# Performance work log

Measured on AMD Instinct MI355X. Metric: run time of the kernel, lower is better.

The kernel has to match this reference:

```python
import jax, jax.numpy as jnp
import numpy as np

N_NODES = 50000
N_EDGES = 600000
D = 128
LN_EPS = 1e-5


def _mlp_ln(x, W1, b1, W2, b2, g, beta):
    # Linear -> ReLU -> Linear -> LayerNorm (standard MeshGraphNets model_fn)
    h = jax.nn.relu(x @ W1 + b1)
    y = h @ W2 + b2
    mu = jnp.mean(y, axis=-1, keepdims=True)
    var = jnp.var(y, axis=-1, keepdims=True)
    return (y - mu) * jax.lax.rsqrt(var + LN_EPS) * g + beta


def setup_inputs() -> dict:
    key = jax.random.key(0)
    ks = jax.random.split(key, 16)
    def glorot(k, shape):
        fan = shape[0] + shape[1]
        return jax.random.normal(k, shape, jnp.float32) * np.sqrt(2.0 / fan)
    inp = {
        "node_features": jax.random.normal(ks[0], (1, N_NODES, D), jnp.float32),
        "edge_features": jax.random.normal(ks[1], (1, N_EDGES, D), jnp.float32),
        "senders": jax.random.randint(ks[2], (N_EDGES,), 0, N_NODES),
        "receivers": jax.random.randint(ks[3], (N_EDGES,), 0, N_NODES),
        # edge MLP: in 3*D -> 128 -> D, LayerNorm
        "eW1": glorot(ks[4], (3 * D, 128)), "eb1": jnp.zeros((128,), jnp.float32),
        "eW2": glorot(ks[5], (128, D)), "eb2": jnp.zeros((D,), jnp.float32),
        "eg": jnp.ones((D,), jnp.float32), "ebeta": jnp.zeros((D,), jnp.float32),
        # node MLP: in 2*D -> 128 -> D, LayerNorm
        "nW1": glorot(ks[6], (2 * D, 128)), "nb1": jnp.zeros((128,), jnp.float32),
        "nW2": glorot(ks[7], (128, D)), "nb2": jnp.zeros((D,), jnp.float32),
        "ng": jnp.ones((D,), jnp.float32), "nbeta": jnp.zeros((D,), jnp.float32),
        # attention linear D -> 1
        "aW": glorot(ks[8], (D, 1)), "ab": jnp.zeros((1,), jnp.float32),
    }
    return inp


def reference(node_features, edge_features, senders, receivers,
              eW1, eb1, eW2, eb2, eg, ebeta,
              nW1, nb1, nW2, nb2, ng, nbeta,
              aW, ab):
    # --- edge update: gather + concat + MLP ---
    sf = node_features[:, senders]      # [1,E,D]
    rf = node_features[:, receivers]    # [1,E,D]
    new_ef = _mlp_ln(jnp.concatenate([sf, rf, edge_features], -1),
                     eW1, eb1, eW2, eb2, eg, ebeta)  # [1,E,D]
    # --- per-edge attention: linear + LeakyReLU + scatter_softmax over receivers ---
    logits = jax.nn.leaky_relu(new_ef @ aW + ab, 0.2)[0, :, 0]  # [E]
    seg_max = jax.ops.segment_max(logits, receivers, num_segments=N_NODES)
    seg_max = jnp.where(jnp.isfinite(seg_max), seg_max, 0.0)
    ex = jnp.exp(logits - seg_max[receivers])
    seg_sum = jax.ops.segment_sum(ex, receivers, num_segments=N_NODES)
    att = ex / seg_sum[receivers]  # [E]
    # --- scatter-add aggregation ---
    agg = jax.ops.segment_sum(new_ef[0] * att[:, None], receivers,
                              num_segments=N_NODES)[None]  # [1,N,D]
    new_nf = _mlp_ln(jnp.concatenate([node_features, agg], -1),
                     nW1, nb1, nW2, nb2, ng, nbeta)  # [1,N,D]
    # residual connections
    new_nf = new_nf + node_features
    new_ef = new_ef + edge_features
    return new_nf, new_ef
```

## Files before the change

### kernel.cpp

```cpp
#include <hip/hip_runtime.h>
#include <hip/hip_bf16.h>

#define N_NODES 50000
#define N_EDGES 600000
#define D 128
#define LN_EPS 1e-5f

typedef float f32x4 __attribute__((ext_vector_type(4)));
typedef int   i32x4 __attribute__((ext_vector_type(4)));
typedef short s16x8 __attribute__((ext_vector_type(8)));

#define W1P_OFF     0u
#define W2P_OFF     98304u
#define NW1P_OFF    131072u
#define NW2P_OFF    196608u
#define SEGKEY_OFF  229376u
#define SEGSUM_OFF  429440u
#define LOGITS_OFF  629504u
#define EX_OFF      3029504u
#define AGG_OFF     5429504u
#define RAW_OFF     31029504u
#define WS_NEED_RAW (RAW_OFF + (size_t)N_EDGES * D * 2)

static __device__ __forceinline__ unsigned short f2bf(float f) {
    unsigned int u = __float_as_uint(f);
    u = (u + 0x7FFFu + ((u >> 16) & 1u)) >> 16;
    return (unsigned short)u;
}
static __device__ __forceinline__ float bf2f(unsigned short h) {
    unsigned int u = ((unsigned int)h) << 16;
    return __uint_as_float(u);
}
static __device__ __forceinline__ int pkbf2(float a, float b) {
    union { __hip_bfloat16 h[2]; int i; } u;
    u.h[0] = __float2bfloat16(a);
    u.h[1] = __float2bfloat16(b);
    return u.i;
}
union frag_u { i32x4 i; s16x8 s; };
static __device__ __forceinline__ unsigned int fkey(float f) {
    unsigned int u = __float_as_uint(f);
    return (u & 0x80000000u) ? ~u : (u | 0x80000000u);
}
static __device__ __forceinline__ float unkey(unsigned int k) {
    unsigned int u = (k & 0x80000000u) ? (k & 0x7FFFFFFFu) : ~k;
    return __uint_as_float(u);
}
static __device__ __forceinline__ f32x4 mfma_bf16(s16x8 a, s16x8 b, f32x4 c) {
    return __builtin_amdgcn_mfma_f32_16x16x32_bf16(a, b, c, 0, 0, 0);
}

__global__ void k_init(const float* __restrict__ eW1, const float* __restrict__ eW2,
                       const float* __restrict__ nW1, const float* __restrict__ nW2,
                       char* __restrict__ ws) {
    int idx = blockIdx.x * 256 + threadIdx.x;
    if (idx < N_NODES * D) ((float*)(ws + AGG_OFF))[idx] = 0.0f;
    if (idx < N_NODES) {
        ((unsigned int*)(ws + SEGKEY_OFF))[idx] = 0u;
        ((float*)(ws + SEGSUM_OFF))[idx] = 0.0f;
    }
    int e = idx & 7, lane = (idx >> 3) & 63, ct = (idx >> 9) & 7, ks = idx >> 12;
    int k = ks * 32 + (lane >> 4) * 8 + e;
    int j = ct * 16 + (lane & 15);
    if (idx < 12 * 4096) ((unsigned short*)(ws + W1P_OFF))[idx]  = f2bf(eW1[k * 128 + j]);
    if (idx < 4 * 4096)  ((unsigned short*)(ws + W2P_OFF))[idx]  = f2bf(eW2[k * 128 + j]);
    if (idx < 8 * 4096)  ((unsigned short*)(ws + NW1P_OFF))[idx] = f2bf(nW1[k * 128 + j]);
    if (idx < 4 * 4096)  ((unsigned short*)(ws + NW2P_OFF))[idx] = f2bf(nW2[k * 128 + j]);
}

template <int STORE_RAW>
__global__ __launch_bounds__(256, 4) void k_edge(
    const float* __restrict__ nf, const float* __restrict__ ef,
    const int* __restrict__ snd, const int* __restrict__ rcv,
    const i32x4* __restrict__ B1, const i32x4* __restrict__ B2,
    const float* __restrict__ b1, const float* __restrict__ b2,
    const float* __restrict__ g, const float* __restrict__ beta,
    const float* __restrict__ aW, const float* __restrict__ ab,
    float* __restrict__ out_ef, float* __restrict__ logits,
    unsigned int* __restrict__ segkey, unsigned short* __restrict__ rawbuf)
{
    __shared__ __align__(16) char  hbuf[64 * 128 * 2];
    __shared__ __align__(16) i32x4 bstage[2][512];
    const int tid = threadIdx.x, lane = tid & 63, rt = tid >> 6;
    const int j0 = lane & 15, hi = lane >> 4;

    const long eA = (long)blockIdx.x * 64 + rt * 16 + j0;
    const int sA = snd[eA], rA = rcv[eA];
    const float* __restrict__ prowS = nf + (size_t)sA * D;
    const float* __restrict__ prowR = nf + (size_t)rA * D;
    const float* __restrict__ prowE = ef + (size_t)eA * D;

    bstage[0][tid]       = B1[tid];
    bstage[0][256 + tid] = B1[256 + tid];
    __syncthreads();

    f32x4 acc[8];
    #pragma unroll
    for (int ct = 0; ct < 8; ++ct) acc[ct] = (f32x4){0.f, 0.f, 0.f, 0.f};
    for (int s = 0; s < 12; ++s) {
        const int cur = s & 1, nxt = cur ^ 1;
        const i32x4* src = (s + 1 < 12) ? (B1 + (s + 1) * 512) : B2;
        i32x4 t0 = src[tid], t1 = src[256 + tid];
        bstage[nxt][tid]       = t0;
        bstage[nxt][256 + tid] = t1;
        const float* p = (s < 4 ? prowS : (s < 8 ? prowR : prowE)) + (s & 3) * 32 + hi * 8;
        float4 f0 = *(const float4*)p;
        float4 f1 = *(const float4*)(p + 4);
        frag_u a;
        a.i[0] = pkbf2(f0.x, f0.y); a.i[1] = pkbf2(f0.z, f0.w);
        a.i[2] = pkbf2(f1.x, f1.y); a.i[3] = pkbf2(f1.z, f1.w);
        #pragma unroll
        for (int ct = 0; ct < 8; ++ct) {
            frag_u b; b.i = bstage[cur][ct * 64 + lane];
            acc[ct] = mfma_bf16(a.s, b.s, acc[ct]);
        }
        __syncthreads();
    }

    #pragma unroll
    for (int ct = 0; ct < 8; ++ct) {
        float bb = b1[ct * 16 + j0];
        #pragma unroll
        for (int rg = 0; rg < 4; ++rg) {
            int row = rt * 16 + hi * 4 + rg;
            float y = fmaxf(acc[ct][rg] + bb, 0.0f);
            int addr = (row * 256 + (ct * 16 + j0) * 2) ^ ((row & 7) << 4);
            *(__hip_bfloat16*)(hbuf + addr) = __float2bfloat16(y);
        }
    }
    asm volatile("" ::: "memory");

    #pragma unroll
    for (int ct = 0; ct < 8; ++ct) acc[ct] = (f32x4){0.f, 0.f, 0.f, 0.f};
    {
        const int arow = rt * 16 + j0;
        for (int s2 = 0; s2 < 4; ++s2) {
            const int cur = (12 + s2) & 1, nxt = cur ^ 1;
            if (s2 < 3) {
                const i32x4* src = B2 + (s2 + 1) * 512;
                i32x4 t0 = src[tid], t1 = src[256 + tid];
                bstage[nxt][tid]       = t0;
                bstage[nxt][256 + tid] = t1;
            }
            int addr = (arow * 256 + (s2 * 32 + hi * 8) * 2) ^ ((arow & 7) << 4);
            frag_u a;
            a.i = *(const i32x4*)(hbuf + addr);
            #pragma unroll
            for (int ct = 0; ct < 8; ++ct) {
                frag_u b; b.i = bstage[cur][ct * 64 + lane];
                acc[ct] = mfma_bf16(a.s, b.s, acc[ct]);
            }
            if (s2 < 3) __syncthreads();
        }
    }

    float b2v[8], gv[8], bv[8], awv[8];
    #pragma unroll
    for (int ct = 0; ct < 8; ++ct) {
        int c = ct * 16 + j0;
        b2v[ct] = b2[c]; gv[ct] = g[c]; bv[ct] = beta[c]; awv[ct] = aW[c];
    }
    float abv = ab[0];
    #pragma unroll
    for (int rg = 0; rg < 4; ++rg) {
        int row = rt * 16 + hi * 4 + rg;
        long e = (long)blockIdx.x * 64 + row;
        float y[8]; float s = 0.f, sq = 0.f;
        #pragma unroll
        for (int ct = 0; ct < 8; ++ct) {
            y[ct] = acc[ct][rg] + b2v[ct];
            s += y[ct]; sq += y[ct] * y[ct];
        }
        #pragma unroll
        for (int m = 1; m <= 8; m <<= 1) { s += __shfl_xor(s, m); sq += __shfl_xor(sq, m); }
        float mu = s * (1.0f / 128.0f);
        float var = sq * (1.0f / 128.0f) - mu * mu;
        float rs = rsqrtf(var + LN_EPS);
        const float* efr = ef + (size_t)e * D;
        float* outr = out_ef + (size_t)e * D;
        unsigned short* rawr = STORE_RAW ? (rawbuf + (size_t)e * D) : nullptr;
        float lg = 0.f;
        #pragma unroll
        for (int ct = 0; ct < 8; ++ct) {
            int c = ct * 16 + j0;
            float o = (y[ct] - mu) * rs * gv[ct] + bv[ct];
            outr[c] = o + efr[c];
            if (STORE_RAW) rawr[c] = f2bf(o);
            lg += o * awv[ct];
        }
        #pragma unroll
        for (int m = 1; m <= 8; m <<= 1) lg += __shfl_xor(lg, m);
        if (j0 == 0) {
            float L = lg + abv;
            L = (L >= 0.f) ? L : 0.2f * L;
            logits[e] = L;
            atomicMax(&segkey[rcv[e]], fkey(L));
        }
    }
}

__global__ void k_exps(const float* __restrict__ logits, const int* __restrict__ rcv,
                       const unsigned int* __restrict__ segkey,
                       float* __restrict__ ex, float* __restrict__ segsum)
{
    int e = blockIdx.x * 256 + threadIdx.x;
    if (e >= N_EDGES) return;
    int r = rcv[e];
    float v = __expf(logits[e] - unkey(segkey[r]));
    ex[e] = v;
    unsafeAtomicAdd(&segsum[r], v);
}

__global__ void k_scatter_raw(const unsigned short* __restrict__ raw,
                              const int* __restrict__ rcv, const float* __restrict__ ex,
                              const float* __restrict__ segsum, float* __restrict__ agg)
{
    long idx = (long)blockIdx.x * 256 + threadIdx.x;
    int e = (int)(idx >> 7);
    int c = (int)(idx & 127);
    int r = rcv[e];
    float att = ex[e] / segsum[r];
    unsafeAtomicAdd(&agg[(size_t)r * D + c], bf2f(raw[idx]) * att);
}

__global__ void k_scatter(const float* __restrict__ out_ef, const float* __restrict__ ef,
                          const int* __restrict__ rcv, const float* __restrict__ ex,
                          const float* __restrict__ segsum, float* __restrict__ agg)
{
    long idx = (long)blockIdx.x * 256 + threadIdx.x;
    int e = (int)(idx >> 7);
    int c = (int)(idx & 127);
    int r = rcv[e];
    float att = ex[e] / segsum[r];
    float raw = out_ef[idx] - ef[idx];
    unsafeAtomicAdd(&agg[(size_t)r * D + c], raw * att);
}

__global__ __launch_bounds__(256, 4) void k_node(
    const float* __restrict__ nf, const float* __restrict__ agg,
    const s16x8* __restrict__ B1, const s16x8* __restrict__ B2,
    const float* __restrict__ b1, const float* __restrict__ b2,
    const float* __restrict__ g, const float* __restrict__ beta,
    float* __restrict__ out_nf)
{
    __shared__ __align__(16) char hbuf[64 * 128 * 2];
    const int tid = threadIdx.x, lane = tid & 63, rt = tid >> 6;
    const int j0 = lane & 15, hi = lane >> 4;

    long nA = (long)blockIdx.x * 64 + rt * 16 + j0;
    if (nA >= N_NODES) nA = 0;
    const float* __restrict__ prowN = nf  + (size_t)nA * D;
    const float* __restrict__ prowA = agg + (size_t)nA * D;

    f32x4 acc[8];
    #pragma unroll
    for (int ct = 0; ct < 8; ++ct) acc[ct] = (f32x4){0.f, 0.f, 0.f, 0.f};
    #pragma unroll
    for (int ks = 0; ks < 8; ++ks) {
        const float* p = (ks < 4 ? prowN : prowA) + (ks & 3) * 32 + hi * 8;
        float4 f0 = *(const float4*)p;
        float4 f1 = *(const float4*)(p + 4);
        frag_u a;
        a.i[0] = pkbf2(f0.x, f0.y); a.i[1] = pkbf2(f0.z, f0.w);
        a.i[2] = pkbf2(f1.x, f1.y); a.i[3] = pkbf2(f1.z, f1.w);
        #pragma unroll
        for (int ct = 0; ct < 8; ++ct)
            acc[ct] = mfma_bf16(a.s, B1[(ks * 8 + ct) * 64 + lane], acc[ct]);
    }

    #pragma unroll
    for (int ct = 0; ct < 8; ++ct) {
        float bb = b1[ct * 16 + j0];
        #pragma unroll
        for (int rg = 0; rg < 4; ++rg) {
            int row = rt * 16 + hi * 4 + rg;
            float y = fmaxf(acc[ct][rg] + bb, 0.0f);
            int addr = (row * 256 + (ct * 16 + j0) * 2) ^ ((row & 7) << 4);
            *(__hip_bfloat16*)(hbuf + addr) = __float2bfloat16(y);
        }
    }
    asm volatile("" ::: "memory");

    #pragma unroll
    for (int ct = 0; ct < 8; ++ct) acc[ct] = (f32x4){0.f, 0.f, 0.f, 0.f};
    {
        int arow = rt * 16 + j0;
        #pragma unroll
        for (int ks = 0; ks < 4; ++ks) {
            int addr = (arow * 256 + (ks * 32 + hi * 8) * 2) ^ ((arow & 7) << 4);
            frag_u a;
            a.i = *(const i32x4*)(hbuf + addr);
            #pragma unroll
            for (int ct = 0; ct < 8; ++ct)
                acc[ct] = mfma_bf16(a.s, B2[(ks * 8 + ct) * 64 + lane], acc[ct]);
        }
    }

    float b2v[8], gv[8], bv[8];
    #pragma unroll
    for (int ct = 0; ct < 8; ++ct) {
        int c = ct * 16 + j0;
        b2v[ct] = b2[c]; gv[ct] = g[c]; bv[ct] = beta[c];
    }
    #pragma unroll
    for (int rg = 0; rg < 4; ++rg) {
        int row = rt * 16 + hi * 4 + rg;
        long n = (long)blockIdx.x * 64 + row;
        float y[8]; float s = 0.f, sq = 0.f;
        #pragma unroll
        for (int ct = 0; ct < 8; ++ct) {
            y[ct] = acc[ct][rg] + b2v[ct];
            s += y[ct]; sq += y[ct] * y[ct];
        }
        #pragma unroll
        for (int m = 1; m <= 8; m <<= 1) { s += __shfl_xor(s, m); sq += __shfl_xor(sq, m); }
        float mu = s * (1.0f / 128.0f);
        float var = sq * (1.0f / 128.0f) - mu * mu;
        float rs = rsqrtf(var + LN_EPS);
        if (n < N_NODES) {
            const float* nfr = nf + (size_t)n * D;
            float* outr = out_nf + (size_t)n * D;
            #pragma unroll
            for (int ct = 0; ct < 8; ++ct) {
                int c = ct * 16 + j0;
                float o = (y[ct] - mu) * rs * gv[ct] + bv[ct];
                outr[c] = o + nfr[c];
            }
        }
    }
}

extern "C" void kernel_launch(void* const* d_in, const int* in_sizes, int n_in,
                              void* d_out, int out_size, void* d_ws, size_t ws_size,
                              hipStream_t stream)
{
    (void)in_sizes; (void)n_in; (void)out_size;
    const float* nf    = (const float*)d_in[0];
    const float* ef    = (const float*)d_in[1];
    const int*   snd   = (const int*)d_in[2];
    const int*   rcv   = (const int*)d_in[3];
    const float* eW1   = (const float*)d_in[4];
    const float* eb1   = (const float*)d_in[5];
    const float* eW2   = (const float*)d_in[6];
    const float* eb2   = (const float*)d_in[7];
    const float* eg    = (const float*)d_in[8];
    const float* ebeta = (const float*)d_in[9];
    const float* nW1   = (const float*)d_in[10];
    const float* nb1   = (const float*)d_in[11];
    const float* nW2   = (const float*)d_in[12];
    const float* nb2   = (const float*)d_in[13];
    const float* ng    = (const float*)d_in[14];
    const float* nbeta = (const float*)d_in[15];
    const float* aW    = (const float*)d_in[16];
    const float* ab    = (const float*)d_in[17];

    float* out_nf = (float*)d_out;
    float* out_ef = out_nf + (size_t)N_NODES * D;
    char*  ws     = (char*)d_ws;

    const bool use_raw = (ws_size >= WS_NEED_RAW);

    k_init<<<25000, 256, 0, stream>>>(eW1, eW2, nW1, nW2, ws);

    if (use_raw) {
        k_edge<1><<<N_EDGES / 64, 256, 0, stream>>>(
            nf, ef, snd, rcv,
            (const i32x4*)(ws + W1P_OFF), (const i32x4*)(ws + W2P_OFF),
            eb1, eb2, eg, ebeta, aW, ab,
            out_ef, (float*)(ws + LOGITS_OFF), (unsigned int*)(ws + SEGKEY_OFF),
            (unsigned short*)(ws + RAW_OFF));
    } else {
        k_edge<0><<<N_EDGES / 64, 256, 0, stream>>>(
            nf, ef, snd, rcv,
            (const i32x4*)(ws + W1P_OFF), (const i32x4*)(ws + W2P_OFF),
            eb1, eb2, eg, ebeta, aW, ab,
            out_ef, (float*)(ws + LOGITS_OFF), (unsigned int*)(ws + SEGKEY_OFF),
            nullptr);
    }

    k_exps<<<(N_EDGES + 255) / 256, 256, 0, stream>>>(
        (const float*)(ws + LOGITS_OFF), rcv, (const unsigned int*)(ws + SEGKEY_OFF),
        (float*)(ws + EX_OFF), (float*)(ws + SEGSUM_OFF));

    if (use_raw) {
        k_scatter_raw<<<(int)(((long)N_EDGES * D) / 256), 256, 0, stream>>>(
            (const unsigned short*)(ws + RAW_OFF), rcv, (const float*)(ws + EX_OFF),
            (const float*)(ws + SEGSUM_OFF), (float*)(ws + AGG_OFF));
    } else {
        k_scatter<<<(int)(((long)N_EDGES * D) / 256), 256, 0, stream>>>(
            out_ef, ef, rcv, (const float*)(ws + EX_OFF),
            (const float*)(ws + SEGSUM_OFF), (float*)(ws + AGG_OFF));
    }

    k_node<<<(N_NODES + 63) / 64, 256, 0, stream>>>(
        nf, (const float*)(ws + AGG_OFF),
        (const s16x8*)(ws + NW1P_OFF), (const s16x8*)(ws + NW2P_OFF),
        nb1, nb2, ng, nbeta, out_nf);
}
```

Baseline: 676.2 us.

## Replace atomic scatter softmax with CSR-by-receiver segmented aggregation

Builds a CSR edge list grouped by receiver (count, single-block scan, fill) each call and replaces the atomicMax, exp/segsum and per-element atomic scatter kernels with one k_agg kernel. In k_agg each wavefront owns a node, computes its max, exp weights and weighted sum of edge features, and writes agg directly. This removes 77M float atomics and the agg zeroing pass. In exchange it adds CSR construction with per-edge atomics, a serial one-block scan, and irregular gathered reads. Accumulation order changes because edges are placed in the list by atomic cursor order.

```diff
diff --git a/kernel.cpp b/kernel.cpp
--- a/kernel.cpp
+++ b/kernel.cpp
@@ -14,12 +14,13 @@
 #define W2P_OFF     98304u
 #define NW1P_OFF    131072u
 #define NW2P_OFF    196608u
-#define SEGKEY_OFF  229376u
-#define SEGSUM_OFF  429440u
+#define DEG_OFF     229376u
+#define ROWPTR_OFF  429440u
 #define LOGITS_OFF  629504u
-#define EX_OFF      3029504u
-#define AGG_OFF     5429504u
-#define RAW_OFF     31029504u
+#define CURSOR_OFF  3029504u
+#define ELIST_OFF   3229504u
+#define AGG_OFF     5629504u
+#define RAW_OFF     31229504u
 #define WS_NEED_RAW (RAW_OFF + (size_t)N_EDGES * D * 2)
 
 static __device__ __forceinline__ unsigned short f2bf(float f) {
@@ -28,8 +29,7 @@
     return (unsigned short)u;
 }
 static __device__ __forceinline__ float bf2f(unsigned short h) {
-    unsigned int u = ((unsigned int)h) << 16;
-    return __uint_as_float(u);
+    return __uint_as_float(((unsigned int)h) << 16);
 }
 static __device__ __forceinline__ int pkbf2(float a, float b) {
     union { __hip_bfloat16 h[2]; int i; } u;
@@ -38,14 +38,6 @@
     return u.i;
 }
 union frag_u { i32x4 i; s16x8 s; };
-static __device__ __forceinline__ unsigned int fkey(float f) {
-    unsigned int u = __float_as_uint(f);
-    return (u & 0x80000000u) ? ~u : (u | 0x80000000u);
-}
-static __device__ __forceinline__ float unkey(unsigned int k) {
-    unsigned int u = (k & 0x80000000u) ? (k & 0x7FFFFFFFu) : ~k;
-    return __uint_as_float(u);
-}
 static __device__ __forceinline__ f32x4 mfma_bf16(s16x8 a, s16x8 b, f32x4 c) {
     return __builtin_amdgcn_mfma_f32_16x16x32_bf16(a, b, c, 0, 0, 0);
 }
@@ -54,10 +46,9 @@
                        const float* __restrict__ nW1, const float* __restrict__ nW2,
                        char* __restrict__ ws) {
     int idx = blockIdx.x * 256 + threadIdx.x;
-    if (idx < N_NODES * D) ((float*)(ws + AGG_OFF))[idx] = 0.0f;
     if (idx < N_NODES) {
-        ((unsigned int*)(ws + SEGKEY_OFF))[idx] = 0u;
-        ((float*)(ws + SEGSUM_OFF))[idx] = 0.0f;
+        ((int*)(ws + DEG_OFF))[idx] = 0;
+        ((int*)(ws + CURSOR_OFF))[idx] = 0;
     }
     int e = idx & 7, lane = (idx >> 3) & 63, ct = (idx >> 9) & 7, ks = idx >> 12;
     int k = ks * 32 + (lane >> 4) * 8 + e;
@@ -66,6 +57,42 @@
     if (idx < 4 * 4096)  ((unsigned short*)(ws + W2P_OFF))[idx]  = f2bf(eW2[k * 128 + j]);
     if (idx < 8 * 4096)  ((unsigned short*)(ws + NW1P_OFF))[idx] = f2bf(nW1[k * 128 + j]);
     if (idx < 4 * 4096)  ((unsigned short*)(ws + NW2P_OFF))[idx] = f2bf(nW2[k * 128 + j]);
+}
+
+__global__ void k_count(const int* __restrict__ rcv, int* __restrict__ deg) {
+    int e = blockIdx.x * 256 + threadIdx.x;
+    if (e < N_EDGES) atomicAdd(&deg[rcv[e]], 1);
+}
+
+__global__ void k_scan(const int* __restrict__ deg, int* __restrict__ rowptr) {
+    __shared__ int part[256];
+    const int tid = threadIdx.x;
+    const int CH = (N_NODES + 255) / 256;
+    const int base = tid * CH;
+    int s = 0;
+    for (int i = 0; i < CH; ++i) { int idx = base + i; if (idx < N_NODES) s += deg[idx]; }
+    part[tid] = s;
+    __syncthreads();
+    if (tid == 0) {
+        int run = 0;
+        for (int j = 0; j < 256; ++j) { int t = part[j]; part[j] = run; run += t; }
+        rowptr[N_NODES] = run;
+    }
+    __syncthreads();
+    int run = part[tid];
+    for (int i = 0; i < CH; ++i) {
+        int idx = base + i;
+        if (idx < N_NODES) { rowptr[idx] = run; run += deg[idx]; }
+    }
+}
+
+__global__ void k_fill(const int* __restrict__ rcv, const int* __restrict__ rowptr,
+                       int* __restrict__ cursor, int* __restrict__ elist) {
+    int e = blockIdx.x * 256 + threadIdx.x;
+    if (e >= N_EDGES) return;
+    int r = rcv[e];
+    int slot = atomicAdd(&cursor[r], 1);
+    elist[rowptr[r] + slot] = e;
 }
 
 template <int STORE_RAW>
@@ -77,7 +104,7 @@
     const float* __restrict__ g, const float* __restrict__ beta,
     const float* __restrict__ aW, const float* __restrict__ ab,
     float* __restrict__ out_ef, float* __restrict__ logits,
-    unsigned int* __restrict__ segkey, unsigned short* __restrict__ rawbuf)
+    unsigned short* __restrict__ rawbuf)
 {
     __shared__ __align__(16) char  hbuf[64 * 128 * 2];
     __shared__ __align__(16) i32x4 bstage[2][512];
@@ -194,46 +221,42 @@
             float L = lg + abv;
             L = (L >= 0.f) ? L : 0.2f * L;
             logits[e] = L;
-            atomicMax(&segkey[rcv[e]], fkey(L));
-        }
-    }
-}
-
-__global__ void k_exps(const float* __restrict__ logits, const int* __restrict__ rcv,
-                       const unsigned int* __restrict__ segkey,
-                       float* __restrict__ ex, float* __restrict__ segsum)
+        }
+    }
+}
+
+template <int USE_RAW>
+__global__ __launch_bounds__(256) void k_agg(
+    const int* __restrict__ rowptr, const int* __restrict__ elist,
+    const float* __restrict__ logits, const unsigned int* __restrict__ raw32,
+    const float* __restrict__ out_ef, const float* __restrict__ ef,
+    float* __restrict__ agg)
 {
-    int e = blockIdx.x * 256 + threadIdx.x;
-    if (e >= N_EDGES) return;
-    int r = rcv[e];
-    float v = __expf(logits[e] - unkey(segkey[r]));
-    ex[e] = v;
-    unsafeAtomicAdd(&segsum[r], v);
-}
-
-__global__ void k_scatter_raw(const unsigned short* __restrict__ raw,
-                              const int* __restrict__ rcv, const float* __restrict__ ex,
-                              const float* __restrict__ segsum, float* __restrict__ agg)
-{
-    long idx = (long)blockIdx.x * 256 + threadIdx.x;
-    int e = (int)(idx >> 7);
-    int c = (int)(idx & 127);
-    int r = rcv[e];
-    float att = ex[e] / segsum[r];
-    unsafeAtomicAdd(&agg[(size_t)r * D + c], bf2f(raw[idx]) * att);
-}
-
-__global__ void k_scatter(const float* __restrict__ out_ef, const float* __restrict__ ef,
-                          const int* __restrict__ rcv, const float* __restrict__ ex,
-                          const float* __restrict__ segsum, float* __restrict__ agg)
-{
-    long idx = (long)blockIdx.x * 256 + threadIdx.x;
-    int e = (int)(idx >> 7);
-    int c = (int)(idx & 127);
-    int r = rcv[e];
-    float att = ex[e] / segsum[r];
-    float raw = out_ef[idx] - ef[idx];
-    unsafeAtomicAdd(&agg[(size_t)r * D + c], raw * att);
+    const int tid = threadIdx.x, lane = tid & 63, w = tid >> 6;
+    const int r = blockIdx.x * 4 + w;
+    const int beg = rowptr[r], end = rowptr[r + 1];
+
+    float mx = -3.4e38f;
+    for (int i = beg; i < end; ++i) mx = fmaxf(mx, logits[elist[i]]);
+
+    float ssum = 0.f, ax = 0.f, ay = 0.f;
+    for (int i = beg; i < end; ++i) {
+        int e = elist[i];
+        float wt = __expf(logits[e] - mx);
+        ssum += wt;
+        if (USE_RAW) {
+            unsigned int u = raw32[(size_t)e * 64 + lane];
+            ax += bf2f((unsigned short)(u & 0xffffu)) * wt;
+            ay += bf2f((unsigned short)(u >> 16)) * wt;
+        } else {
+            float2 o = ((const float2*)out_ef)[(size_t)e * 64 + lane];
+            float2 f = ((const float2*)ef)[(size_t)e * 64 + lane];
+            ax += (o.x - f.x) * wt;
+            ay += (o.y - f.y) * wt;
+        }
+    }
+    float inv = (ssum > 0.f) ? 1.0f / ssum : 0.0f;
+    ((float2*)agg)[(size_t)r * 64 + lane] = make_float2(ax * inv, ay * inv);
 }
 
 __global__ __launch_bounds__(256, 4) void k_node(
@@ -360,36 +383,33 @@
 
     const bool use_raw = (ws_size >= WS_NEED_RAW);
 
-    k_init<<<25000, 256, 0, stream>>>(eW1, eW2, nW1, nW2, ws);
+    k_init<<<196, 256, 0, stream>>>(eW1, eW2, nW1, nW2, ws);
+
+    k_count<<<(N_EDGES + 255) / 256, 256, 0, stream>>>(rcv, (int*)(ws + DEG_OFF));
+    k_scan<<<1, 256, 0, stream>>>((const int*)(ws + DEG_OFF), (int*)(ws + ROWPTR_OFF));
+    k_fill<<<(N_EDGES + 255) / 256, 256, 0, stream>>>(
+        rcv, (const int*)(ws + ROWPTR_OFF), (int*)(ws + CURSOR_OFF), (int*)(ws + ELIST_OFF));
 
     if (use_raw) {
         k_edge<1><<<N_EDGES / 64, 256, 0, stream>>>(
             nf, ef, snd, rcv,
             (const i32x4*)(ws + W1P_OFF), (const i32x4*)(ws + W2P_OFF),
             eb1, eb2, eg, ebeta, aW, ab,
-            out_ef, (float*)(ws + LOGITS_OFF), (unsigned int*)(ws + SEGKEY_OFF),
-            (unsigned short*)(ws + RAW_OFF));
+            out_ef, (float*)(ws + LOGITS_OFF), (unsigned short*)(ws + RAW_OFF));
+        k_agg<1><<<N_NODES / 4, 256, 0, stream>>>(
+            (const int*)(ws + ROWPTR_OFF), (const int*)(ws + ELIST_OFF),
+            (const float*)(ws + LOGITS_OFF), (const unsigned int*)(ws + RAW_OFF),
+            nullptr, nullptr, (float*)(ws + AGG_OFF));
     } else {
         k_edge<0><<<N_EDGES / 64, 256, 0, stream>>>(
             nf, ef, snd, rcv,
             (const i32x4*)(ws + W1P_OFF), (const i32x4*)(ws + W2P_OFF),
             eb1, eb2, eg, ebeta, aW, ab,
-            out_ef, (float*)(ws + LOGITS_OFF), (unsigned int*)(ws + SEGKEY_OFF),
-            nullptr);
-    }
-
-    k_exps<<<(N_EDGES + 255) / 256, 256, 0, stream>>>(
-        (const float*)(ws + LOGITS_OFF), rcv, (const unsigned int*)(ws + SEGKEY_OFF),
-        (float*)(ws + EX_OFF), (float*)(ws + SEGSUM_OFF));
-
-    if (use_raw) {
-        k_scatter_raw<<<(int)(((long)N_EDGES * D) / 256), 256, 0, stream>>>(
-            (const unsigned short*)(ws + RAW_OFF), rcv, (const float*)(ws + EX_OFF),
-            (const float*)(ws + SEGSUM_OFF), (float*)(ws + AGG_OFF));
-    } else {
-        k_scatter<<<(int)(((long)N_EDGES * D) / 256), 256, 0, stream>>>(
-            out_ef, ef, rcv, (const float*)(ws + EX_OFF),
-            (const float*)(ws + SEGSUM_OFF), (float*)(ws + AGG_OFF));
+            out_ef, (float*)(ws + LOGITS_OFF), nullptr);
+        k_agg<0><<<N_NODES / 4, 256, 0, stream>>>(
+            (const int*)(ws + ROWPTR_OFF), (const int*)(ws + ELIST_OFF),
+            (const float*)(ws + LOGITS_OFF), nullptr,
+            out_ef, ef, (float*)(ws + AGG_OFF));
     }
 
     k_node<<<(N_NODES + 63) / 64, 256, 0, stream>>>(
```

After: 653.6 us. 1.03x faster.
